# Kernel optimization log

Measured on AMD Instinct MI355X. Metric: run time of the kernel, lower is better.

The kernel has to match this reference:

```python
import jax, jax.numpy as jnp
import numpy as np

BATCH, NODE, IN_DIM, DIM, TOPK = 256, 256, 64, 64, 20
EPS = 1e-5
NEG_SLOPE = 0.2


def setup_inputs() -> dict:
    key = jax.random.key(0)
    ks = jax.random.split(key, 10)
    z, o = jnp.zeros, jnp.ones
    return {
        "data": jax.random.normal(ks[0], (BATCH, NODE, IN_DIM), jnp.float32),
        "emb_table": jax.random.normal(ks[1], (NODE, DIM), jnp.float32) * 0.1,
        "lin_w": jax.random.normal(ks[2], (IN_DIM, DIM), jnp.float32) * 0.05,
        "att_i": jax.random.normal(ks[3], (DIM,), jnp.float32) * 0.1,
        "att_j": jax.random.normal(ks[4], (DIM,), jnp.float32) * 0.1,
        "att_em_i": jax.random.normal(ks[5], (DIM,), jnp.float32) * 0.1,
        "att_em_j": jax.random.normal(ks[6], (DIM,), jnp.float32) * 0.1,
        "gnn_bias": z((DIM,), jnp.float32),
        "bn1_gamma": o((DIM,), jnp.float32), "bn1_beta": z((DIM,), jnp.float32),
        "bn2_gamma": o((DIM,), jnp.float32), "bn2_beta": z((DIM,), jnp.float32),
        "enc_w": jax.random.normal(ks[7], (NODE * DIM, DIM), jnp.float32) * 0.01,
        "enc_b": z((DIM,), jnp.float32),
        "arr_w": jax.random.normal(ks[8], (DIM, 7), jnp.float32) * 0.1,
        "arr_b": z((7,), jnp.float32),
        "out_w": jax.random.normal(ks[9], (DIM, 1), jnp.float32) * 0.1,
        "out_b": z((1,), jnp.float32),
    }


def _batchnorm(x, gamma, beta, axes):
    # BatchNorm1d in training mode: batch statistics
    mean = jnp.mean(x, axis=axes, keepdims=True)
    var = jnp.var(x, axis=axes, keepdims=True)
    return (x - mean) * jax.lax.rsqrt(var + EPS) * gamma + beta


def _gdn_forward(data, emb_table, lin_w, att_i, att_j, att_em_i, att_em_j, gnn_bias,
                 bn1_gamma, bn1_beta, bn2_gamma, bn2_beta,
                 enc_w, enc_b, arr_w, arr_b, out_w, out_b):
    B, N, F = data.shape
    BN = B * N
    x = data.reshape(BN, F)

    # learned graph: top-k cosine similarity of (detached) node embeddings
    w = jax.lax.stop_gradient(emb_table)
    nrm = jnp.linalg.norm(w, axis=-1)
    cos = (w @ w.T) / (nrm[:, None] * nrm[None, :])
    topk_idx = jax.lax.top_k(cos, TOPK)[1]                 # [N, TOPK]

    # gated_edge_index = (gated_j=sources, gated_i=targets), batched with +b*N offset
    src1 = topk_idx.reshape(-1)                            # sources (j)
    dst1 = jnp.repeat(jnp.arange(N), TOPK)                 # targets (i)
    offs = (jnp.arange(B) * N)[:, None]
    src = (src1[None, :] + offs).reshape(-1)               # [B*N*TOPK]
    dst = (dst1[None, :] + offs).reshape(-1)

    # PyG: remove_self_loops then add_self_loops -> mask duplicate self edges,
    # append exactly one self loop per node
    loop = jnp.arange(BN)
    src_all = jnp.concatenate([src, loop])
    dst_all = jnp.concatenate([dst, loop])
    valid = jnp.concatenate([src != dst, jnp.ones((BN,), bool)])

    # GraphLayer (GAT-style, heads=1, concat=False)
    xl = x @ lin_w                                         # [BN, DIM]
    emb_rep = jnp.tile(emb_table, (B, 1))                  # [BN, DIM] (embedding.repeat(B,1))
    x_i, x_j = xl[dst_all], xl[src_all]                    # per-edge gathers
    e_i, e_j = emb_rep[dst_all], emb_rep[src_all]
    logits = (x_i @ att_i) + (e_i @ att_em_i) + (x_j @ att_j) + (e_j @ att_em_j)
    logits = jnp.where(logits >= 0, logits, NEG_SLOPE * logits)  # leaky_relu(0.2)
    logits = jnp.where(valid, logits, -1e9)

    # segment softmax over incoming edges of each target node
    seg_max = jax.ops.segment_max(logits, dst_all, num_segments=BN)
    a = jnp.where(valid, jnp.exp(logits - seg_max[dst_all]), 0.0)
    denom = jax.ops.segment_sum(a, dst_all, num_segments=BN)
    alpha = a / denom[dst_all]

    # weighted scatter-add aggregation + bias, then GNNLayer BN + ReLU
    agg = jax.ops.segment_sum(x_j * alpha[:, None], dst_all, num_segments=BN) + gnn_bias
    gnn_out = jax.nn.relu(_batchnorm(agg, bn1_gamma, bn1_beta, axes=(0,)))

    x3 = gnn_out.reshape(B, N, -1)                         # [B, N, DIM]
    encoded = x3.reshape(B, -1) @ enc_w + enc_b            # [B, DIM]
    arrangement = encoded @ arr_w + arr_b                  # [B, 7]

    y = x3 * emb_table[None]                               # mul by node embeddings
    y = jnp.transpose(y, (0, 2, 1))                        # [B, DIM, N]
    y = jax.nn.relu(_batchnorm(y, bn2_gamma[None, :, None], bn2_beta[None, :, None], axes=(0, 2)))
    y = jnp.transpose(y, (0, 2, 1))                        # [B, N, DIM] (dropout is identity in eval)
    score = (y @ out_w + out_b).reshape(B, N)              # OutLayer (layer_num=1) + view(-1, N)
    return score, arrangement


def reference(data, emb_table, lin_w, att_i, att_j, att_em_i, att_em_j, gnn_bias,
              bn1_gamma, bn1_beta, bn2_gamma, bn2_beta,
              enc_w, enc_b, arr_w, arr_b, out_w, out_b):
    return _gdn_forward(data, emb_table, lin_w, att_i, att_j, att_em_i, att_em_j, gnn_bias,
                        bn1_gamma, bn1_beta, bn2_gamma, bn2_beta,
                        enc_w, enc_b, arr_w, arr_b, out_w, out_b)
```

## Files before the change

### kernel.cpp

```cpp
#include <hip/hip_runtime.h>
#include <hip/hip_bf16.h>

#define TK 20
#define BN 65536

typedef const float* fpc;
typedef __attribute__((ext_vector_type(8))) short short8;
typedef __attribute__((ext_vector_type(4))) float floatx4;

__device__ __forceinline__ short f2b(float f){
  unsigned u = __float_as_uint(f);
  return (short)((u + 0x7fffu + ((u >> 16) & 1u)) >> 16);
}
__device__ __forceinline__ float b2fu(unsigned short u){
  return __uint_as_float(((unsigned)u) << 16);
}

__global__ void __launch_bounds__(256) k_gx(fpc data, fpc emb, fpc lin_w, fpc att_i, fpc att_j,
        fpc att_em_i, fpc att_em_j,
        int* __restrict__ topk, float* __restrict__ emi, float* __restrict__ emj,
        __hip_bfloat16* __restrict__ xl, float* __restrict__ aip, float* __restrict__ ajp,
        float* __restrict__ bnsum){
  __shared__ float s_cos[256];
  __shared__ float s_wi[64];
  const int t = threadIdx.x, w = t >> 6, lane = t & 63;

  if (blockIdx.x < 256){
    if (blockIdx.x == 0){
      #pragma unroll
      for (int i = 0; i < 8; ++i) bnsum[t + i*256] = 0.f;
    }
    const int i = blockIdx.x;
    if (t < 64) s_wi[t] = emb[i*64 + t];
    __syncthreads();
    float dot = 0.f, nj = 0.f, ni = 0.f;
    for (int f = 0; f < 64; ++f){
      float wj = emb[t*64 + f], wi = s_wi[f];
      dot = fmaf(wi, wj, dot); nj = fmaf(wj, wj, nj); ni = fmaf(wi, wi, ni);
    }
    s_cos[t] = dot / (sqrtf(ni) * sqrtf(nj));
    __syncthreads();
    if (t < 64){
      float v0 = s_cos[t], v1 = s_cos[t+64], v2 = s_cos[t+128], v3 = s_cos[t+192];
      int taken = 0;
      for (int r = 0; r < TK; ++r){
        float bv = (taken & 1) ? -3.f : v0; int bi = t;
        float c;
        c = (taken & 2) ? -3.f : v1; if (c > bv){ bv = c; bi = t+64;  }
        c = (taken & 4) ? -3.f : v2; if (c > bv){ bv = c; bi = t+128; }
        c = (taken & 8) ? -3.f : v3; if (c > bv){ bv = c; bi = t+192; }
        for (int m = 1; m < 64; m <<= 1){
          float ov = __shfl_xor(bv, m, 64);
          int   oi = __shfl_xor(bi, m, 64);
          if (ov > bv || (ov == bv && oi < bi)){ bv = ov; bi = oi; }
        }
        if (t == 0) topk[i*TK + r] = bi;
        if ((bi & 63) == t) taken |= 1 << (bi >> 6);
      }
    } else if (t < 128){
      int d = t - 64;
      float wv = s_wi[d];
      float p1 = wv * att_em_i[d];
      float p2 = wv * att_em_j[d];
      for (int m = 1; m < 64; m <<= 1){
        p1 += __shfl_xor(p1, m, 64);
        p2 += __shfl_xor(p2, m, 64);
      }
      if (d == 0){ emi[i] = p1; emj[i] = p2; }
    }
    return;
  }

  const int m = lane & 15, quad = lane >> 4;
  short8 B[4][2];
  #pragma unroll
  for (int ct = 0; ct < 4; ++ct)
    #pragma unroll
    for (int kc = 0; kc < 2; ++kc)
      #pragma unroll
      for (int j = 0; j < 8; ++j)
        B[ct][kc][j] = f2b(lin_w[(kc*32 + quad*8 + j)*64 + ct*16 + m]);

  const int rw = (blockIdx.x - 256)*64 + w*16;
  short8 A0, A1;
  {
    const float4* ap0 = (const float4*)(data + (size_t)(rw + m)*64 + quad*8);
    float4 q0 = ap0[0], q1 = ap0[1];
    A0[0]=f2b(q0.x); A0[1]=f2b(q0.y); A0[2]=f2b(q0.z); A0[3]=f2b(q0.w);
    A0[4]=f2b(q1.x); A0[5]=f2b(q1.y); A0[6]=f2b(q1.z); A0[7]=f2b(q1.w);
    const float4* ap1 = (const float4*)(data + (size_t)(rw + m)*64 + 32 + quad*8);
    float4 q2 = ap1[0], q3 = ap1[1];
    A1[0]=f2b(q2.x); A1[1]=f2b(q2.y); A1[2]=f2b(q2.z); A1[3]=f2b(q2.w);
    A1[4]=f2b(q3.x); A1[5]=f2b(q3.y); A1[6]=f2b(q3.z); A1[7]=f2b(q3.w);
  }
  floatx4 acc[4];
  #pragma unroll
  for (int ct = 0; ct < 4; ++ct){
    floatx4 z = {0.f, 0.f, 0.f, 0.f};
    acc[ct] = __builtin_amdgcn_mfma_f32_16x16x32_bf16(A0, B[ct][0], z, 0, 0, 0);
    acc[ct] = __builtin_amdgcn_mfma_f32_16x16x32_bf16(A1, B[ct][1], acc[ct], 0, 0, 0);
  }
  float p1[4] = {0.f,0.f,0.f,0.f}, p2[4] = {0.f,0.f,0.f,0.f};
  #pragma unroll
  for (int ct = 0; ct < 4; ++ct){
    const float wi = att_i[ct*16 + m], wj = att_j[ct*16 + m];
    #pragma unroll
    for (int reg = 0; reg < 4; ++reg){
      float v = acc[ct][reg];
      const int row = rw + quad*4 + reg;
      xl[(size_t)row*64 + ct*16 + m] = __float2bfloat16(v);
      p1[reg] = fmaf(v, wi, p1[reg]);
      p2[reg] = fmaf(v, wj, p2[reg]);
    }
  }
  #pragma unroll
  for (int reg = 0; reg < 4; ++reg){
    #pragma unroll
    for (int s = 1; s < 16; s <<= 1){
      p1[reg] += __shfl_xor(p1[reg], s, 16);
      p2[reg] += __shfl_xor(p2[reg], s, 16);
    }
    if (m == 0){
      const int r = rw + quad*4 + reg;
      aip[r] = p1[reg];
      ajp[r] = p2[reg];
    }
  }
}

__global__ void __launch_bounds__(256) k_attn_agg(const int* __restrict__ topk,
                         const __hip_bfloat16* __restrict__ xl,
                         fpc aip, fpc ajp, fpc emi_g, fpc emj_g, fpc gnn_bias,
                         __hip_bfloat16* __restrict__ agg, float* __restrict__ bnsum){
  __shared__ float s_alpha[4][32];
  __shared__ int   s_src[4][32];
  __shared__ float s_ps[4][64], s_pq[4][64];
  const int t = threadIdx.x, w = t >> 6, lane = t & 63;
  const float bias = gnn_bias[lane];
  const int vbase = blockIdx.x*64 + w*16;
  float sum = 0.f, sq = 0.f;
  for (int j = 0; j < 16; ++j){
    const int v = vbase + j, i = v & 255, b = v >> 8;
    float lg = -1e30f; int sl = 0;
    if (lane < 21){
      sl = (lane < 20) ? topk[i*TK + lane] : i;
      if (lane == 20 || sl != i){
        float l = aip[v] + emi_g[i] + ajp[b*256 + sl] + emj_g[sl];
        lg = (l >= 0.f) ? l : 0.2f*l;
      }
    }
    float m = lg;
    for (int s = 1; s < 32; s <<= 1) m = fmaxf(m, __shfl_xor(m, s, 32));
    float e = (lg > -1e29f) ? __expf(lg - m) : 0.f;
    float den = e;
    for (int s = 1; s < 32; s <<= 1) den += __shfl_xor(den, s, 32);
    if (lane < 21){ s_alpha[w][lane] = e / den; s_src[w][lane] = b*256 + sl; }
    float acc = bias;
    #pragma unroll
    for (int k = 0; k < 21; ++k)
      acc = fmaf(s_alpha[w][k], __bfloat162float(xl[(size_t)s_src[w][k]*64 + lane]), acc);
    agg[(size_t)v*64 + lane] = __float2bfloat16(acc);
    sum += acc; sq = fmaf(acc, acc, sq);
  }
  s_ps[w][lane] = sum; s_pq[w][lane] = sq;
  __syncthreads();
  if (t < 64){
    const int cp = (blockIdx.x & 7)*64;
    atomicAdd(&bnsum[cp + t],       s_ps[0][t] + s_ps[1][t] + s_ps[2][t] + s_ps[3][t]);
    atomicAdd(&bnsum[512 + cp + t], s_pq[0][t] + s_pq[1][t] + s_pq[2][t] + s_pq[3][t]);
  }
}

__global__ void __launch_bounds__(256) k_encst(const __hip_bfloat16* __restrict__ agg, fpc enc_w,
                         fpc emb, fpc g1, fpc be1,
                         float* __restrict__ bnsum, float* __restrict__ part){
  const int t = threadIdx.x;

  if (blockIdx.x < 256){
    const int w = t >> 6, lane = t & 63;
    const int m = lane & 15, quad = lane >> 4;
    const int kt = blockIdx.x & 127, bt = blockIdx.x >> 7, kbase = kt*128;
    float scA[8], shA[8], scB[8], shB[8];
    #pragma unroll
    for (int j = 0; j < 8; ++j){
      #pragma unroll
      for (int par = 0; par < 2; ++par){
        const int d = par*32 + quad*8 + j;
        float S = 0.f, Q = 0.f;
        #pragma unroll
        for (int cp = 0; cp < 8; ++cp){ S += bnsum[cp*64 + d]; Q += bnsum[512 + cp*64 + d]; }
        float mean = S * (1.f/BN);
        float var  = Q * (1.f/BN) - mean*mean;
        float sc = g1[d] * rsqrtf(var + 1e-5f);
        float sh = be1[d] - mean*sc;
        if (par == 0){ scA[j] = sc; shA[j] = sh; } else { scB[j] = sc; shB[j] = sh; }
      }
    }
    floatx4 acc[2][4];
    #pragma unroll
    for (int i = 0; i < 2; ++i)
      #pragma unroll
      for (int ct = 0; ct < 4; ++ct)
        acc[i][ct] = (floatx4){0.f, 0.f, 0.f, 0.f};

    #pragma unroll
    for (int kc = 0; kc < 4; ++kc){
      const int kof = kbase + kc*32 + quad*8;
      const bool odd = (kc & 1);
      short8 Bf[4];
      #pragma unroll
      for (int ct = 0; ct < 4; ++ct)
        #pragma unroll
        for (int j = 0; j < 8; ++j)
          Bf[ct][j] = f2b(enc_w[(size_t)(kof + j)*64 + ct*16 + m]);
      #pragma unroll
      for (int i = 0; i < 2; ++i){
        const int row = bt*128 + (w*2 + i)*16 + m;
        uint4 uu = *(const uint4*)((const unsigned short*)agg + (size_t)row*16384 + kof);
        unsigned short h[8] = {
          (unsigned short)(uu.x & 0xffff), (unsigned short)(uu.x >> 16),
          (unsigned short)(uu.y & 0xffff), (unsigned short)(uu.y >> 16),
          (unsigned short)(uu.z & 0xffff), (unsigned short)(uu.z >> 16),
          (unsigned short)(uu.w & 0xffff), (unsigned short)(uu.w >> 16) };
        short8 Af;
        if (!odd){
          #pragma unroll
          for (int j = 0; j < 8; ++j) Af[j] = f2b(fmaxf(fmaf(b2fu(h[j]), scA[j], shA[j]), 0.f));
        } else {
          #pragma unroll
          for (int j = 0; j < 8; ++j) Af[j] = f2b(fmaxf(fmaf(b2fu(h[j]), scB[j], shB[j]), 0.f));
        }
        #pragma unroll
        for (int ct = 0; ct < 4; ++ct)
          acc[i][ct] = __builtin_amdgcn_mfma_f32_16x16x32_bf16(Af, Bf[ct], acc[i][ct], 0, 0, 0);
      }
    }
    #pragma unroll
    for (int i = 0; i < 2; ++i)
      #pragma unroll
      for (int ct = 0; ct < 4; ++ct)
        #pragma unroll
        for (int reg = 0; reg < 4; ++reg){
          const int row = bt*128 + (w*2 + i)*16 + quad*4 + reg;
          part[(size_t)kt*16384 + row*64 + ct*16 + m] = acc[i][ct][reg];
        }
    return;
  }

  const int sb = blockIdx.x - 256;
  const int qc = t & 15, rs = t >> 4;
  float4 sc, sh;
  {
    float s[4], q[4];
    #pragma unroll
    for (int k = 0; k < 4; ++k){
      const int d = qc*4 + k;
      float S = 0.f, Q = 0.f;
      #pragma unroll
      for (int cp = 0; cp < 8; ++cp){ S += bnsum[cp*64 + d]; Q += bnsum[512 + cp*64 + d]; }
      float mean = S * (1.f/BN);
      float var  = Q * (1.f/BN) - mean*mean;
      s[k] = g1[d] * rsqrtf(var + 1e-5f);
      q[k] = be1[d] - mean*s[k];
    }
    sc = make_float4(s[0], s[1], s[2], s[3]);
    sh = make_float4(q[0], q[1], q[2], q[3]);
  }
  const float4* emb4 = (const float4*)emb;
  float4 ys = make_float4(0,0,0,0), yq = make_float4(0,0,0,0);
  const int rbase = sb*32;
  #pragma unroll
  for (int jj = 0; jj < 2; ++jj){
    const int r = rbase + jj*16 + rs;
    ushort4 u = *(const ushort4*)((const unsigned short*)agg + (size_t)r*64 + qc*4);
    float4 e = emb4[(r & 255)*16 + qc];
    float4 y;
    y.x = fmaxf(fmaf(b2fu(u.x), sc.x, sh.x), 0.f) * e.x;
    y.y = fmaxf(fmaf(b2fu(u.y), sc.y, sh.y), 0.f) * e.y;
    y.z = fmaxf(fmaf(b2fu(u.z), sc.z, sh.z), 0.f) * e.z;
    y.w = fmaxf(fmaf(b2fu(u.w), sc.w, sh.w), 0.f) * e.w;
    ys.x += y.x; ys.y += y.y; ys.z += y.z; ys.w += y.w;
    yq.x = fmaf(y.x, y.x, yq.x); yq.y = fmaf(y.y, y.y, yq.y);
    yq.z = fmaf(y.z, y.z, yq.z); yq.w = fmaf(y.w, y.w, yq.w);
  }
  __shared__ float4 s_s[16][16], s_q[16][16];
  s_s[rs][qc] = ys; s_q[rs][qc] = yq;
  __syncthreads();
  if (t < 64){
    const int qq = t >> 2, comp = t & 3;
    float S = 0.f, Q = 0.f;
    #pragma unroll
    for (int rr = 0; rr < 16; ++rr){
      S += ((const float*)&s_s[rr][qq])[comp];
      Q += ((const float*)&s_q[rr][qq])[comp];
    }
    const int cp = (sb & 7)*64;
    atomicAdd(&bnsum[1024 + cp + t], S);
    atomicAdd(&bnsum[1536 + cp + t], Q);
  }
}

__global__ void __launch_bounds__(256) k_fin(const float* __restrict__ part,
                      const __hip_bfloat16* __restrict__ agg, fpc emb,
                      fpc g1, fpc be1, fpc g2, fpc be2,
                      const float* __restrict__ bnsum,
                      fpc enc_b, fpc arr_w, fpc arr_b, fpc out_w, fpc out_b,
                      float* __restrict__ out){
  const int t = threadIdx.x;

  if (blockIdx.x < 256){
    __shared__ float s_enc[4][64];
    const int b = blockIdx.x, w = t >> 6, lane = t & 63;
    float s = 0.f;
    #pragma unroll 8
    for (int k = 0; k < 32; ++k)
      s += part[(size_t)(w*32 + k)*16384 + b*64 + lane];
    s_enc[w][lane] = s;
    __syncthreads();
    if (t < 64){
      float e = s_enc[0][t] + s_enc[1][t] + s_enc[2][t] + s_enc[3][t] + enc_b[t];
      float o[7];
      #pragma unroll
      for (int j = 0; j < 7; ++j) o[j] = e * arr_w[t*7 + j];
      #pragma unroll
      for (int j = 0; j < 7; ++j)
        #pragma unroll
        for (int m = 1; m < 64; m <<= 1) o[j] += __shfl_xor(o[j], m, 64);
      if (t == 0){
        #pragma unroll
        for (int j = 0; j < 7; ++j) out[65536 + b*7 + j] = o[j] + arr_b[j];
      }
    }
    return;
  }

  const int w = t >> 6, lane = t & 63;
  const int qc = lane & 15, rq = lane >> 4;
  float sc1[4], sh1[4], sc2[4], sh2[4], ow[4];
  #pragma unroll
  for (int k = 0; k < 4; ++k){
    const int d = qc*4 + k;
    float S1 = 0.f, Q1 = 0.f, S2 = 0.f, Q2 = 0.f;
    #pragma unroll
    for (int cp = 0; cp < 8; ++cp){
      S1 += bnsum[cp*64 + d];        Q1 += bnsum[512 + cp*64 + d];
      S2 += bnsum[1024 + cp*64 + d]; Q2 += bnsum[1536 + cp*64 + d];
    }
    float m1 = S1 * (1.f/BN), v1 = Q1 * (1.f/BN) - m1*m1;
    sc1[k] = g1[d] * rsqrtf(v1 + 1e-5f);
    sh1[k] = be1[d] - m1*sc1[k];
    float m2 = S2 * (1.f/BN), v2 = Q2 * (1.f/BN) - m2*m2;
    sc2[k] = g2[d] * rsqrtf(v2 + 1e-5f);
    sh2[k] = be2[d] - m2*sc2[k];
    ow[k]  = out_w[d];
  }
  const float ob = out_b[0];
  const float4* emb4 = (const float4*)emb;
  const int base = (blockIdx.x - 256)*32 + w*8;
  #pragma unroll
  for (int it = 0; it < 2; ++it){
    const int r = base + it*4 + rq;
    ushort4 u = *(const ushort4*)((const unsigned short*)agg + (size_t)r*64 + qc*4);
    float4 e4 = emb4[(r & 255)*16 + qc];
    float p = 0.f, g, y, yh;
    g = fmaxf(fmaf(b2fu(u.x), sc1[0], sh1[0]), 0.f); y = g*e4.x;
    yh = fmaxf(fmaf(y, sc2[0], sh2[0]), 0.f); p = fmaf(yh, ow[0], p);
    g = fmaxf(fmaf(b2fu(u.y), sc1[1], sh1[1]), 0.f); y = g*e4.y;
    yh = fmaxf(fmaf(y, sc2[1], sh2[1]), 0.f); p = fmaf(yh, ow[1], p);
    g = fmaxf(fmaf(b2fu(u.z), sc1[2], sh1[2]), 0.f); y = g*e4.z;
    yh = fmaxf(fmaf(y, sc2[2], sh2[2]), 0.f); p = fmaf(yh, ow[2], p);
    g = fmaxf(fmaf(b2fu(u.w), sc1[3], sh1[3]), 0.f); y = g*e4.w;
    yh = fmaxf(fmaf(y, sc2[3], sh2[3]), 0.f); p = fmaf(yh, ow[3], p);
    #pragma unroll
    for (int mm = 1; mm < 16; mm <<= 1) p += __shfl_xor(p, mm, 16);
    if (qc == 0) out[r] = p + ob;
  }
}

extern "C" void kernel_launch(void* const* d_in, const int* in_sizes, int n_in,
                              void* d_out, int out_size, void* d_ws, size_t ws_size,
                              hipStream_t stream) {
  fpc data     = (fpc)d_in[0];
  fpc emb      = (fpc)d_in[1];
  fpc lin_w    = (fpc)d_in[2];
  fpc att_i    = (fpc)d_in[3];
  fpc att_j    = (fpc)d_in[4];
  fpc att_em_i = (fpc)d_in[5];
  fpc att_em_j = (fpc)d_in[6];
  fpc gnn_bias = (fpc)d_in[7];
  fpc g1       = (fpc)d_in[8];
  fpc be1      = (fpc)d_in[9];
  fpc g2       = (fpc)d_in[10];
  fpc be2      = (fpc)d_in[11];
  fpc enc_w    = (fpc)d_in[12];
  fpc enc_b    = (fpc)d_in[13];
  fpc arr_w    = (fpc)d_in[14];
  fpc arr_b    = (fpc)d_in[15];
  fpc out_w    = (fpc)d_in[16];
  fpc out_b    = (fpc)d_in[17];

  float* fw = (float*)d_ws;
  int*   topk    = (int*)d_ws;
  float* emi     = fw + 5120;
  float* emj     = fw + 5376;
  float* bnsum   = fw + 5632;
  float* aip     = fw + 7680;
  float* ajp     = fw + 73216;
  __hip_bfloat16* agg = (__hip_bfloat16*)(fw + 138752);
  __hip_bfloat16* xl  = (__hip_bfloat16*)(fw + 2235904);
  float* part    = (float*)xl;
  float* out     = (float*)d_out;

  k_gx       <<<1280,  256, 0, stream>>>(data, emb, lin_w, att_i, att_j, att_em_i, att_em_j,
                                         topk, emi, emj, xl, aip, ajp, bnsum);
  k_attn_agg <<<1024,  256, 0, stream>>>(topk, xl, aip, ajp, emi, emj, gnn_bias, agg, bnsum);
  k_encst    <<<2304,  256, 0, stream>>>(agg, enc_w, emb, g1, be1, bnsum, part);
  k_fin      <<<2304,  256, 0, stream>>>(part, agg, emb, g1, be1, g2, be2, bnsum,
                                         enc_b, arr_w, arr_b, out_w, out_b, out);
}
```

Measured before the change: 174.4 us.

## Fuse four kernels into one persistent kernel with grid-wide barriers

```diff
diff --git a/kernel.cpp b/kernel.cpp
--- a/kernel.cpp
+++ b/kernel.cpp
@@ -3,6 +3,7 @@
 
 #define TK 20
 #define BN 65536
+#define NB 512
 
 typedef const float* fpc;
 typedef __attribute__((ext_vector_type(8))) short short8;
@@ -16,26 +17,49 @@
   return __uint_as_float(((unsigned)u) << 16);
 }
 
-__global__ void __launch_bounds__(256) k_gx(fpc data, fpc emb, fpc lin_w, fpc att_i, fpc att_j,
-        fpc att_em_i, fpc att_em_j,
-        int* __restrict__ topk, float* __restrict__ emi, float* __restrict__ emj,
-        __hip_bfloat16* __restrict__ xl, float* __restrict__ aip, float* __restrict__ ajp,
-        float* __restrict__ bnsum){
+struct KP {
+  const float *data, *emb, *lin_w, *att_i, *att_j, *att_em_i, *att_em_j,
+              *gnn_bias, *g1, *be1, *g2, *be2, *enc_w, *enc_b, *arr_w, *arr_b,
+              *out_w, *out_b;
+  int *topk;
+  float *emi, *emj, *bnsum;
+  unsigned *bar;
+  float *aip, *ajp;
+  __hip_bfloat16 *agg, *xl;
+  float *part, *out;
+};
+
+__device__ __forceinline__ void gbar(unsigned* bar, unsigned target){
+  __syncthreads();
+  if (threadIdx.x == 0){
+    __threadfence();
+    __hip_atomic_fetch_add(bar, 1u, __ATOMIC_RELEASE, __HIP_MEMORY_SCOPE_AGENT);
+    while (__hip_atomic_load(bar, __ATOMIC_ACQUIRE, __HIP_MEMORY_SCOPE_AGENT) < target)
+      __builtin_amdgcn_s_sleep(8);
+    __threadfence();
+  }
+  __syncthreads();
+}
+
+__global__ void __launch_bounds__(256, 2) mega(KP p){
+  const int t = threadIdx.x, w = t >> 6, lane = t & 63;
+  const int m = lane & 15, quad = lane >> 4;
+
   __shared__ float s_cos[256];
   __shared__ float s_wi[64];
-  const int t = threadIdx.x, w = t >> 6, lane = t & 63;
+  __shared__ float s_alpha[4][32];
+  __shared__ int   s_src[4][32];
+  __shared__ float s_ps[4][64], s_pq[4][64];
+  __shared__ float4 s_s[16][16], s_q[16][16];
+  __shared__ float s_enc[4][64];
 
   if (blockIdx.x < 256){
-    if (blockIdx.x == 0){
-      #pragma unroll
-      for (int i = 0; i < 8; ++i) bnsum[t + i*256] = 0.f;
-    }
     const int i = blockIdx.x;
-    if (t < 64) s_wi[t] = emb[i*64 + t];
+    if (t < 64) s_wi[t] = p.emb[i*64 + t];
     __syncthreads();
     float dot = 0.f, nj = 0.f, ni = 0.f;
     for (int f = 0; f < 64; ++f){
-      float wj = emb[t*64 + f], wi = s_wi[f];
+      float wj = p.emb[t*64 + f], wi = s_wi[f];
       dot = fmaf(wi, wj, dot); nj = fmaf(wj, wj, nj); ni = fmaf(wi, wi, ni);
     }
     s_cos[t] = dot / (sqrtf(ni) * sqrtf(nj));
@@ -49,136 +73,125 @@
         c = (taken & 2) ? -3.f : v1; if (c > bv){ bv = c; bi = t+64;  }
         c = (taken & 4) ? -3.f : v2; if (c > bv){ bv = c; bi = t+128; }
         c = (taken & 8) ? -3.f : v3; if (c > bv){ bv = c; bi = t+192; }
-        for (int m = 1; m < 64; m <<= 1){
-          float ov = __shfl_xor(bv, m, 64);
-          int   oi = __shfl_xor(bi, m, 64);
+        for (int mm = 1; mm < 64; mm <<= 1){
+          float ov = __shfl_xor(bv, mm, 64);
+          int   oi = __shfl_xor(bi, mm, 64);
           if (ov > bv || (ov == bv && oi < bi)){ bv = ov; bi = oi; }
         }
-        if (t == 0) topk[i*TK + r] = bi;
+        if (t == 0) p.topk[i*TK + r] = bi;
         if ((bi & 63) == t) taken |= 1 << (bi >> 6);
       }
     } else if (t < 128){
       int d = t - 64;
       float wv = s_wi[d];
-      float p1 = wv * att_em_i[d];
-      float p2 = wv * att_em_j[d];
-      for (int m = 1; m < 64; m <<= 1){
-        p1 += __shfl_xor(p1, m, 64);
-        p2 += __shfl_xor(p2, m, 64);
-      }
-      if (d == 0){ emi[i] = p1; emj[i] = p2; }
-    }
-    return;
-  }
-
-  const int m = lane & 15, quad = lane >> 4;
-  short8 B[4][2];
-  #pragma unroll
-  for (int ct = 0; ct < 4; ++ct)
-    #pragma unroll
-    for (int kc = 0; kc < 2; ++kc)
-      #pragma unroll
-      for (int j = 0; j < 8; ++j)
-        B[ct][kc][j] = f2b(lin_w[(kc*32 + quad*8 + j)*64 + ct*16 + m]);
-
-  const int rw = (blockIdx.x - 256)*64 + w*16;
-  short8 A0, A1;
+      float p1 = wv * p.att_em_i[d];
+      float p2 = wv * p.att_em_j[d];
+      for (int mm = 1; mm < 64; mm <<= 1){
+        p1 += __shfl_xor(p1, mm, 64);
+        p2 += __shfl_xor(p2, mm, 64);
+      }
+      if (d == 0){ p.emi[i] = p1; p.emj[i] = p2; }
+    }
+    __syncthreads();
+  }
   {
-    const float4* ap0 = (const float4*)(data + (size_t)(rw + m)*64 + quad*8);
-    float4 q0 = ap0[0], q1 = ap0[1];
-    A0[0]=f2b(q0.x); A0[1]=f2b(q0.y); A0[2]=f2b(q0.z); A0[3]=f2b(q0.w);
-    A0[4]=f2b(q1.x); A0[5]=f2b(q1.y); A0[6]=f2b(q1.z); A0[7]=f2b(q1.w);
-    const float4* ap1 = (const float4*)(data + (size_t)(rw + m)*64 + 32 + quad*8);
-    float4 q2 = ap1[0], q3 = ap1[1];
-    A1[0]=f2b(q2.x); A1[1]=f2b(q2.y); A1[2]=f2b(q2.z); A1[3]=f2b(q2.w);
-    A1[4]=f2b(q3.x); A1[5]=f2b(q3.y); A1[6]=f2b(q3.z); A1[7]=f2b(q3.w);
-  }
-  floatx4 acc[4];
-  #pragma unroll
-  for (int ct = 0; ct < 4; ++ct){
-    floatx4 z = {0.f, 0.f, 0.f, 0.f};
-    acc[ct] = __builtin_amdgcn_mfma_f32_16x16x32_bf16(A0, B[ct][0], z, 0, 0, 0);
-    acc[ct] = __builtin_amdgcn_mfma_f32_16x16x32_bf16(A1, B[ct][1], acc[ct], 0, 0, 0);
-  }
-  float p1[4] = {0.f,0.f,0.f,0.f}, p2[4] = {0.f,0.f,0.f,0.f};
-  #pragma unroll
-  for (int ct = 0; ct < 4; ++ct){
-    const float wi = att_i[ct*16 + m], wj = att_j[ct*16 + m];
-    #pragma unroll
-    for (int reg = 0; reg < 4; ++reg){
-      float v = acc[ct][reg];
-      const int row = rw + quad*4 + reg;
-      xl[(size_t)row*64 + ct*16 + m] = __float2bfloat16(v);
-      p1[reg] = fmaf(v, wi, p1[reg]);
-      p2[reg] = fmaf(v, wj, p2[reg]);
-    }
-  }
-  #pragma unroll
-  for (int reg = 0; reg < 4; ++reg){
-    #pragma unroll
-    for (int s = 1; s < 16; s <<= 1){
-      p1[reg] += __shfl_xor(p1[reg], s, 16);
-      p2[reg] += __shfl_xor(p2[reg], s, 16);
-    }
-    if (m == 0){
-      const int r = rw + quad*4 + reg;
-      aip[r] = p1[reg];
-      ajp[r] = p2[reg];
-    }
-  }
-}
-
-__global__ void __launch_bounds__(256) k_attn_agg(const int* __restrict__ topk,
-                         const __hip_bfloat16* __restrict__ xl,
-                         fpc aip, fpc ajp, fpc emi_g, fpc emj_g, fpc gnn_bias,
-                         __hip_bfloat16* __restrict__ agg, float* __restrict__ bnsum){
-  __shared__ float s_alpha[4][32];
-  __shared__ int   s_src[4][32];
-  __shared__ float s_ps[4][64], s_pq[4][64];
-  const int t = threadIdx.x, w = t >> 6, lane = t & 63;
-  const float bias = gnn_bias[lane];
-  const int vbase = blockIdx.x*64 + w*16;
-  float sum = 0.f, sq = 0.f;
-  for (int j = 0; j < 16; ++j){
-    const int v = vbase + j, i = v & 255, b = v >> 8;
-    float lg = -1e30f; int sl = 0;
-    if (lane < 21){
-      sl = (lane < 20) ? topk[i*TK + lane] : i;
-      if (lane == 20 || sl != i){
-        float l = aip[v] + emi_g[i] + ajp[b*256 + sl] + emj_g[sl];
-        lg = (l >= 0.f) ? l : 0.2f*l;
-      }
-    }
-    float m = lg;
-    for (int s = 1; s < 32; s <<= 1) m = fmaxf(m, __shfl_xor(m, s, 32));
-    float e = (lg > -1e29f) ? __expf(lg - m) : 0.f;
-    float den = e;
-    for (int s = 1; s < 32; s <<= 1) den += __shfl_xor(den, s, 32);
-    if (lane < 21){ s_alpha[w][lane] = e / den; s_src[w][lane] = b*256 + sl; }
-    float acc = bias;
-    #pragma unroll
-    for (int k = 0; k < 21; ++k)
-      acc = fmaf(s_alpha[w][k], __bfloat162float(xl[(size_t)s_src[w][k]*64 + lane]), acc);
-    agg[(size_t)v*64 + lane] = __float2bfloat16(acc);
-    sum += acc; sq = fmaf(acc, acc, sq);
-  }
-  s_ps[w][lane] = sum; s_pq[w][lane] = sq;
-  __syncthreads();
-  if (t < 64){
-    const int cp = (blockIdx.x & 7)*64;
-    atomicAdd(&bnsum[cp + t],       s_ps[0][t] + s_ps[1][t] + s_ps[2][t] + s_ps[3][t]);
-    atomicAdd(&bnsum[512 + cp + t], s_pq[0][t] + s_pq[1][t] + s_pq[2][t] + s_pq[3][t]);
-  }
-}
-
-__global__ void __launch_bounds__(256) k_encst(const __hip_bfloat16* __restrict__ agg, fpc enc_w,
-                         fpc emb, fpc g1, fpc be1,
-                         float* __restrict__ bnsum, float* __restrict__ part){
-  const int t = threadIdx.x;
-
-  if (blockIdx.x < 256){
-    const int w = t >> 6, lane = t & 63;
-    const int m = lane & 15, quad = lane >> 4;
+    short8 B[4][2];
+    #pragma unroll
+    for (int ct = 0; ct < 4; ++ct)
+      #pragma unroll
+      for (int kc = 0; kc < 2; ++kc)
+        #pragma unroll
+        for (int j = 0; j < 8; ++j)
+          B[ct][kc][j] = f2b(p.lin_w[(kc*32 + quad*8 + j)*64 + ct*16 + m]);
+    #pragma unroll
+    for (int pass = 0; pass < 2; ++pass){
+      const int rw = blockIdx.x*128 + pass*64 + w*16;
+      short8 A0, A1;
+      {
+        const float4* ap0 = (const float4*)(p.data + (size_t)(rw + m)*64 + quad*8);
+        float4 q0 = ap0[0], q1 = ap0[1];
+        A0[0]=f2b(q0.x); A0[1]=f2b(q0.y); A0[2]=f2b(q0.z); A0[3]=f2b(q0.w);
+        A0[4]=f2b(q1.x); A0[5]=f2b(q1.y); A0[6]=f2b(q1.z); A0[7]=f2b(q1.w);
+        const float4* ap1 = (const float4*)(p.data + (size_t)(rw + m)*64 + 32 + quad*8);
+        float4 q2 = ap1[0], q3 = ap1[1];
+        A1[0]=f2b(q2.x); A1[1]=f2b(q2.y); A1[2]=f2b(q2.z); A1[3]=f2b(q2.w);
+        A1[4]=f2b(q3.x); A1[5]=f2b(q3.y); A1[6]=f2b(q3.z); A1[7]=f2b(q3.w);
+      }
+      floatx4 acc[4];
+      #pragma unroll
+      for (int ct = 0; ct < 4; ++ct){
+        floatx4 z = {0.f, 0.f, 0.f, 0.f};
+        acc[ct] = __builtin_amdgcn_mfma_f32_16x16x32_bf16(A0, B[ct][0], z, 0, 0, 0);
+        acc[ct] = __builtin_amdgcn_mfma_f32_16x16x32_bf16(A1, B[ct][1], acc[ct], 0, 0, 0);
+      }
+      float p1[4] = {0.f,0.f,0.f,0.f}, p2[4] = {0.f,0.f,0.f,0.f};
+      #pragma unroll
+      for (int ct = 0; ct < 4; ++ct){
+        const float wi = p.att_i[ct*16 + m], wj = p.att_j[ct*16 + m];
+        #pragma unroll
+        for (int reg = 0; reg < 4; ++reg){
+          float v = acc[ct][reg];
+          const int row = rw + quad*4 + reg;
+          p.xl[(size_t)row*64 + ct*16 + m] = __float2bfloat16(v);
+          p1[reg] = fmaf(v, wi, p1[reg]);
+          p2[reg] = fmaf(v, wj, p2[reg]);
+        }
+      }
+      #pragma unroll
+      for (int reg = 0; reg < 4; ++reg){
+        #pragma unroll
+        for (int s = 1; s < 16; s <<= 1){
+          p1[reg] += __shfl_xor(p1[reg], s, 16);
+          p2[reg] += __shfl_xor(p2[reg], s, 16);
+        }
+        if (m == 0){
+          const int r = rw + quad*4 + reg;
+          p.aip[r] = p1[reg];
+          p.ajp[r] = p2[reg];
+        }
+      }
+    }
+  }
+  gbar(p.bar, NB);
+
+  {
+    const float bias = p.gnn_bias[lane];
+    const int vbase = blockIdx.x*128 + w*32;
+    float sum = 0.f, sq = 0.f;
+    for (int j = 0; j < 32; ++j){
+      const int v = vbase + j, i = v & 255, b = v >> 8;
+      float lg = -1e30f; int sl = 0;
+      if (lane < 21){
+        sl = (lane < 20) ? p.topk[i*TK + lane] : i;
+        if (lane == 20 || sl != i){
+          float l = p.aip[v] + p.emi[i] + p.ajp[b*256 + sl] + p.emj[sl];
+          lg = (l >= 0.f) ? l : 0.2f*l;
+        }
+      }
+      float mx = lg;
+      for (int s = 1; s < 32; s <<= 1) mx = fmaxf(mx, __shfl_xor(mx, s, 32));
+      float e = (lg > -1e29f) ? __expf(lg - mx) : 0.f;
+      float den = e;
+      for (int s = 1; s < 32; s <<= 1) den += __shfl_xor(den, s, 32);
+      if (lane < 21){ s_alpha[w][lane] = e / den; s_src[w][lane] = b*256 + sl; }
+      float acc = bias;
+      #pragma unroll
+      for (int k = 0; k < 21; ++k)
+        acc = fmaf(s_alpha[w][k], __bfloat162float(p.xl[(size_t)s_src[w][k]*64 + lane]), acc);
+      p.agg[(size_t)v*64 + lane] = __float2bfloat16(acc);
+      sum += acc; sq = fmaf(acc, acc, sq);
+    }
+    s_ps[w][lane] = sum; s_pq[w][lane] = sq;
+    __syncthreads();
+    if (t < 64){
+      const int cp = (blockIdx.x & 7)*64;
+      atomicAdd(&p.bnsum[cp + t],       s_ps[0][t] + s_ps[1][t] + s_ps[2][t] + s_ps[3][t]);
+      atomicAdd(&p.bnsum[512 + cp + t], s_pq[0][t] + s_pq[1][t] + s_pq[2][t] + s_pq[3][t]);
+    }
+  }
+  gbar(p.bar, 2*NB);
+
+  {
     const int kt = blockIdx.x & 127, bt = blockIdx.x >> 7, kbase = kt*128;
     float scA[8], shA[8], scB[8], shB[8];
     #pragma unroll
@@ -188,21 +201,17 @@
         const int d = par*32 + quad*8 + j;
         float S = 0.f, Q = 0.f;
         #pragma unroll
-        for (int cp = 0; cp < 8; ++cp){ S += bnsum[cp*64 + d]; Q += bnsum[512 + cp*64 + d]; }
+        for (int cp = 0; cp < 8; ++cp){ S += p.bnsum[cp*64 + d]; Q += p.bnsum[512 + cp*64 + d]; }
         float mean = S * (1.f/BN);
         float var  = Q * (1.f/BN) - mean*mean;
-        float sc = g1[d] * rsqrtf(var + 1e-5f);
-        float sh = be1[d] - mean*sc;
+        float sc = p.g1[d] * rsqrtf(var + 1e-5f);
+        float sh = p.be1[d] - mean*sc;
         if (par == 0){ scA[j] = sc; shA[j] = sh; } else { scB[j] = sc; shB[j] = sh; }
       }
     }
-    floatx4 acc[2][4];
-    #pragma unroll
-    for (int i = 0; i < 2; ++i)
-      #pragma unroll
-      for (int ct = 0; ct < 4; ++ct)
-        acc[i][ct] = (floatx4){0.f, 0.f, 0.f, 0.f};
-
+    floatx4 acc[4];
+    #pragma unroll
+    for (int ct = 0; ct < 4; ++ct) acc[ct] = (floatx4){0.f, 0.f, 0.f, 0.f};
     #pragma unroll
     for (int kc = 0; kc < 4; ++kc){
       const int kof = kbase + kc*32 + quad*8;
@@ -212,209 +221,191 @@
       for (int ct = 0; ct < 4; ++ct)
         #pragma unroll
         for (int j = 0; j < 8; ++j)
-          Bf[ct][j] = f2b(enc_w[(size_t)(kof + j)*64 + ct*16 + m]);
-      #pragma unroll
-      for (int i = 0; i < 2; ++i){
-        const int row = bt*128 + (w*2 + i)*16 + m;
-        uint4 uu = *(const uint4*)((const unsigned short*)agg + (size_t)row*16384 + kof);
-        unsigned short h[8] = {
-          (unsigned short)(uu.x & 0xffff), (unsigned short)(uu.x >> 16),
-          (unsigned short)(uu.y & 0xffff), (unsigned short)(uu.y >> 16),
-          (unsigned short)(uu.z & 0xffff), (unsigned short)(uu.z >> 16),
-          (unsigned short)(uu.w & 0xffff), (unsigned short)(uu.w >> 16) };
-        short8 Af;
-        if (!odd){
-          #pragma unroll
-          for (int j = 0; j < 8; ++j) Af[j] = f2b(fmaxf(fmaf(b2fu(h[j]), scA[j], shA[j]), 0.f));
-        } else {
-          #pragma unroll
-          for (int j = 0; j < 8; ++j) Af[j] = f2b(fmaxf(fmaf(b2fu(h[j]), scB[j], shB[j]), 0.f));
-        }
-        #pragma unroll
-        for (int ct = 0; ct < 4; ++ct)
-          acc[i][ct] = __builtin_amdgcn_mfma_f32_16x16x32_bf16(Af, Bf[ct], acc[i][ct], 0, 0, 0);
-      }
-    }
-    #pragma unroll
-    for (int i = 0; i < 2; ++i)
+          Bf[ct][j] = f2b(p.enc_w[(size_t)(kof + j)*64 + ct*16 + m]);
+      const int row = bt*64 + w*16 + m;
+      uint4 uu = *(const uint4*)((const unsigned short*)p.agg + (size_t)row*16384 + kof);
+      unsigned short h[8] = {
+        (unsigned short)(uu.x & 0xffff), (unsigned short)(uu.x >> 16),
+        (unsigned short)(uu.y & 0xffff), (unsigned short)(uu.y >> 16),
+        (unsigned short)(uu.z & 0xffff), (unsigned short)(uu.z >> 16),
+        (unsigned short)(uu.w & 0xffff), (unsigned short)(uu.w >> 16) };
+      short8 Af;
+      if (!odd){
+        #pragma unroll
+        for (int j = 0; j < 8; ++j) Af[j] = f2b(fmaxf(fmaf(b2fu(h[j]), scA[j], shA[j]), 0.f));
+      } else {
+        #pragma unroll
+        for (int j = 0; j < 8; ++j) Af[j] = f2b(fmaxf(fmaf(b2fu(h[j]), scB[j], shB[j]), 0.f));
+      }
       #pragma unroll
       for (int ct = 0; ct < 4; ++ct)
-        #pragma unroll
-        for (int reg = 0; reg < 4; ++reg){
-          const int row = bt*128 + (w*2 + i)*16 + quad*4 + reg;
-          part[(size_t)kt*16384 + row*64 + ct*16 + m] = acc[i][ct][reg];
-        }
-    return;
-  }
-
-  const int sb = blockIdx.x - 256;
-  const int qc = t & 15, rs = t >> 4;
-  float4 sc, sh;
+        acc[ct] = __builtin_amdgcn_mfma_f32_16x16x32_bf16(Af, Bf[ct], acc[ct], 0, 0, 0);
+    }
+    #pragma unroll
+    for (int ct = 0; ct < 4; ++ct)
+      #pragma unroll
+      for (int reg = 0; reg < 4; ++reg){
+        const int row = bt*64 + w*16 + quad*4 + reg;
+        p.part[(size_t)kt*16384 + row*64 + ct*16 + m] = acc[ct][reg];
+      }
+  }
   {
-    float s[4], q[4];
-    #pragma unroll
-    for (int k = 0; k < 4; ++k){
-      const int d = qc*4 + k;
+    const int qc = t & 15, rs = t >> 4;
+    float4 sc, sh;
+    {
+      float s[4], q[4];
+      #pragma unroll
+      for (int k = 0; k < 4; ++k){
+        const int d = qc*4 + k;
+        float S = 0.f, Q = 0.f;
+        #pragma unroll
+        for (int cp = 0; cp < 8; ++cp){ S += p.bnsum[cp*64 + d]; Q += p.bnsum[512 + cp*64 + d]; }
+        float mean = S * (1.f/BN);
+        float var  = Q * (1.f/BN) - mean*mean;
+        s[k] = p.g1[d] * rsqrtf(var + 1e-5f);
+        q[k] = p.be1[d] - mean*s[k];
+      }
+      sc = make_float4(s[0], s[1], s[2], s[3]);
+      sh = make_float4(q[0], q[1], q[2], q[3]);
+    }
+    const float4* emb4 = (const float4*)p.emb;
+    float4 ys = make_float4(0,0,0,0), yq = make_float4(0,0,0,0);
+    const int rbase = blockIdx.x*128;
+    #pragma unroll
+    for (int jj = 0; jj < 8; ++jj){
+      const int r = rbase + jj*16 + rs;
+      ushort4 u = *(const ushort4*)((const unsigned short*)p.agg + (size_t)r*64 + qc*4);
+      float4 e = emb4[(r & 255)*16 + qc];
+      float4 y;
+      y.x = fmaxf(fmaf(b2fu(u.x), sc.x, sh.x), 0.f) * e.x;
+      y.y = fmaxf(fmaf(b2fu(u.y), sc.y, sh.y), 0.f) * e.y;
+      y.z = fmaxf(fmaf(b2fu(u.z), sc.z, sh.z), 0.f) * e.z;
+      y.w = fmaxf(fmaf(b2fu(u.w), sc.w, sh.w), 0.f) * e.w;
+      ys.x += y.x; ys.y += y.y; ys.z += y.z; ys.w += y.w;
+      yq.x = fmaf(y.x, y.x, yq.x); yq.y = fmaf(y.y, y.y, yq.y);
+      yq.z = fmaf(y.z, y.z, yq.z); yq.w = fmaf(y.w, y.w, yq.w);
+    }
+    s_s[rs][qc] = ys; s_q[rs][qc] = yq;
+    __syncthreads();
+    if (t < 64){
+      const int qq = t >> 2, comp = t & 3;
       float S = 0.f, Q = 0.f;
       #pragma unroll
-      for (int cp = 0; cp < 8; ++cp){ S += bnsum[cp*64 + d]; Q += bnsum[512 + cp*64 + d]; }
-      float mean = S * (1.f/BN);
-      float var  = Q * (1.f/BN) - mean*mean;
-      s[k] = g1[d] * rsqrtf(var + 1e-5f);
-      q[k] = be1[d] - mean*s[k];
-    }
-    sc = make_float4(s[0], s[1], s[2], s[3]);
-    sh = make_float4(q[0], q[1], q[2], q[3]);
-  }
-  const float4* emb4 = (const float4*)emb;
-  float4 ys = make_float4(0,0,0,0), yq = make_float4(0,0,0,0);
-  const int rbase = sb*32;
-  #pragma unroll
-  for (int jj = 0; jj < 2; ++jj){
-    const int r = rbase + jj*16 + rs;
-    ushort4 u = *(const ushort4*)((const unsigned short*)agg + (size_t)r*64 + qc*4);
-    float4 e = emb4[(r & 255)*16 + qc];
-    float4 y;
-    y.x = fmaxf(fmaf(b2fu(u.x), sc.x, sh.x), 0.f) * e.x;
-    y.y = fmaxf(fmaf(b2fu(u.y), sc.y, sh.y), 0.f) * e.y;
-    y.z = fmaxf(fmaf(b2fu(u.z), sc.z, sh.z), 0.f) * e.z;
-    y.w = fmaxf(fmaf(b2fu(u.w), sc.w, sh.w), 0.f) * e.w;
-    ys.x += y.x; ys.y += y.y; ys.z += y.z; ys.w += y.w;
-    yq.x = fmaf(y.x, y.x, yq.x); yq.y = fmaf(y.y, y.y, yq.y);
-    yq.z = fmaf(y.z, y.z, yq.z); yq.w = fmaf(y.w, y.w, yq.w);
-  }
-  __shared__ float4 s_s[16][16], s_q[16][16];
-  s_s[rs][qc] = ys; s_q[rs][qc] = yq;
-  __syncthreads();
-  if (t < 64){
-    const int qq = t >> 2, comp = t & 3;
-    float S = 0.f, Q = 0.f;
-    #pragma unroll
-    for (int rr = 0; rr < 16; ++rr){
-      S += ((const float*)&s_s[rr][qq])[comp];
-      Q += ((const float*)&s_q[rr][qq])[comp];
-    }
-    const int cp = (sb & 7)*64;
-    atomicAdd(&bnsum[1024 + cp + t], S);
-    atomicAdd(&bnsum[1536 + cp + t], Q);
-  }
-}
-
-__global__ void __launch_bounds__(256) k_fin(const float* __restrict__ part,
-                      const __hip_bfloat16* __restrict__ agg, fpc emb,
-                      fpc g1, fpc be1, fpc g2, fpc be2,
-                      const float* __restrict__ bnsum,
-                      fpc enc_b, fpc arr_w, fpc arr_b, fpc out_w, fpc out_b,
-                      float* __restrict__ out){
-  const int t = threadIdx.x;
+      for (int rr = 0; rr < 16; ++rr){
+        S += ((const float*)&s_s[rr][qq])[comp];
+        Q += ((const float*)&s_q[rr][qq])[comp];
+      }
+      const int cp = (blockIdx.x & 7)*64;
+      atomicAdd(&p.bnsum[1024 + cp + t], S);
+      atomicAdd(&p.bnsum[1536 + cp + t], Q);
+    }
+  }
+  gbar(p.bar, 3*NB);
 
   if (blockIdx.x < 256){
-    __shared__ float s_enc[4][64];
-    const int b = blockIdx.x, w = t >> 6, lane = t & 63;
+    const int b = blockIdx.x;
     float s = 0.f;
     #pragma unroll 8
     for (int k = 0; k < 32; ++k)
-      s += part[(size_t)(w*32 + k)*16384 + b*64 + lane];
+      s += p.part[(size_t)(w*32 + k)*16384 + b*64 + lane];
     s_enc[w][lane] = s;
     __syncthreads();
     if (t < 64){
-      float e = s_enc[0][t] + s_enc[1][t] + s_enc[2][t] + s_enc[3][t] + enc_b[t];
+      float e = s_enc[0][t] + s_enc[1][t] + s_enc[2][t] + s_enc[3][t] + p.enc_b[t];
       float o[7];
       #pragma unroll
-      for (int j = 0; j < 7; ++j) o[j] = e * arr_w[t*7 + j];
+      for (int j = 0; j < 7; ++j) o[j] = e * p.arr_w[t*7 + j];
       #pragma unroll
       for (int j = 0; j < 7; ++j)
         #pragma unroll
-        for (int m = 1; m < 64; m <<= 1) o[j] += __shfl_xor(o[j], m, 64);
+        for (int mm = 1; mm < 64; mm <<= 1) o[j] += __shfl_xor(o[j], mm, 64);
       if (t == 0){
         #pragma unroll
-        for (int j = 0; j < 7; ++j) out[65536 + b*7 + j] = o[j] + arr_b[j];
-      }
-    }
-    return;
-  }
-
-  const int w = t >> 6, lane = t & 63;
-  const int qc = lane & 15, rq = lane >> 4;
-  float sc1[4], sh1[4], sc2[4], sh2[4], ow[4];
-  #pragma unroll
-  for (int k = 0; k < 4; ++k){
-    const int d = qc*4 + k;
-    float S1 = 0.f, Q1 = 0.f, S2 = 0.f, Q2 = 0.f;
-    #pragma unroll
-    for (int cp = 0; cp < 8; ++cp){
-      S1 += bnsum[cp*64 + d];        Q1 += bnsum[512 + cp*64 + d];
-      S2 += bnsum[1024 + cp*64 + d]; Q2 += bnsum[1536 + cp*64 + d];
-    }
-    float m1 = S1 * (1.f/BN), v1 = Q1 * (1.f/BN) - m1*m1;
-    sc1[k] = g1[d] * rsqrtf(v1 + 1e-5f);
-    sh1[k] = be1[d] - m1*sc1[k];
-    float m2 = S2 * (1.f/BN), v2 = Q2 * (1.f/BN) - m2*m2;
-    sc2[k] = g2[d] * rsqrtf(v2 + 1e-5f);
-    sh2[k] = be2[d] - m2*sc2[k];
-    ow[k]  = out_w[d];
-  }
-  const float ob = out_b[0];
-  const float4* emb4 = (const float4*)emb;
-  const int base = (blockIdx.x - 256)*32 + w*8;
-  #pragma unroll
-  for (int it = 0; it < 2; ++it){
-    const int r = base + it*4 + rq;
-    ushort4 u = *(const ushort4*)((const unsigned short*)agg + (size_t)r*64 + qc*4);
-    float4 e4 = emb4[(r & 255)*16 + qc];
-    float p = 0.f, g, y, yh;
-    g = fmaxf(fmaf(b2fu(u.x), sc1[0], sh1[0]), 0.f); y = g*e4.x;
-    yh = fmaxf(fmaf(y, sc2[0], sh2[0]), 0.f); p = fmaf(yh, ow[0], p);
-    g = fmaxf(fmaf(b2fu(u.y), sc1[1], sh1[1]), 0.f); y = g*e4.y;
-    yh = fmaxf(fmaf(y, sc2[1], sh2[1]), 0.f); p = fmaf(yh, ow[1], p);
-    g = fmaxf(fmaf(b2fu(u.z), sc1[2], sh1[2]), 0.f); y = g*e4.z;
-    yh = fmaxf(fmaf(y, sc2[2], sh2[2]), 0.f); p = fmaf(yh, ow[2], p);
-    g = fmaxf(fmaf(b2fu(u.w), sc1[3], sh1[3]), 0.f); y = g*e4.w;
-    yh = fmaxf(fmaf(y, sc2[3], sh2[3]), 0.f); p = fmaf(yh, ow[3], p);
-    #pragma unroll
-    for (int mm = 1; mm < 16; mm <<= 1) p += __shfl_xor(p, mm, 16);
-    if (qc == 0) out[r] = p + ob;
+        for (int j = 0; j < 7; ++j) p.out[65536 + b*7 + j] = o[j] + p.arr_b[j];
+      }
+    }
+    __syncthreads();
+  }
+  {
+    const int qc = lane & 15, rq = lane >> 4;
+    float sc1[4], sh1[4], sc2[4], sh2[4], ow[4];
+    #pragma unroll
+    for (int k = 0; k < 4; ++k){
+      const int d = qc*4 + k;
+      float S1 = 0.f, Q1 = 0.f, S2 = 0.f, Q2 = 0.f;
+      #pragma unroll
+      for (int cp = 0; cp < 8; ++cp){
+        S1 += p.bnsum[cp*64 + d];        Q1 += p.bnsum[512 + cp*64 + d];
+        S2 += p.bnsum[1024 + cp*64 + d]; Q2 += p.bnsum[1536 + cp*64 + d];
+      }
+      float m1 = S1 * (1.f/BN), v1 = Q1 * (1.f/BN) - m1*m1;
+      sc1[k] = p.g1[d] * rsqrtf(v1 + 1e-5f);
+      sh1[k] = p.be1[d] - m1*sc1[k];
+      float m2 = S2 * (1.f/BN), v2 = Q2 * (1.f/BN) - m2*m2;
+      sc2[k] = p.g2[d] * rsqrtf(v2 + 1e-5f);
+      sh2[k] = p.be2[d] - m2*sc2[k];
+      ow[k]  = p.out_w[d];
+    }
+    const float ob = p.out_b[0];
+    const float4* emb4 = (const float4*)p.emb;
+    const int base = blockIdx.x*128 + w*32;
+    #pragma unroll
+    for (int it = 0; it < 8; ++it){
+      const int r = base + it*4 + rq;
+      ushort4 u = *(const ushort4*)((const unsigned short*)p.agg + (size_t)r*64 + qc*4);
+      float4 e4 = emb4[(r & 255)*16 + qc];
+      float pr = 0.f, g, y, yh;
+      g = fmaxf(fmaf(b2fu(u.x), sc1[0], sh1[0]), 0.f); y = g*e4.x;
+      yh = fmaxf(fmaf(y, sc2[0], sh2[0]), 0.f); pr = fmaf(yh, ow[0], pr);
+      g = fmaxf(fmaf(b2fu(u.y), sc1[1], sh1[1]), 0.f); y = g*e4.y;
+      yh = fmaxf(fmaf(y, sc2[1], sh2[1]), 0.f); pr = fmaf(yh, ow[1], pr);
+      g = fmaxf(fmaf(b2fu(u.z), sc1[2], sh1[2]), 0.f); y = g*e4.z;
+      yh = fmaxf(fmaf(y, sc2[2], sh2[2]), 0.f); pr = fmaf(yh, ow[2], pr);
+      g = fmaxf(fmaf(b2fu(u.w), sc1[3], sh1[3]), 0.f); y = g*e4.w;
+      yh = fmaxf(fmaf(y, sc2[3], sh2[3]), 0.f); pr = fmaf(yh, ow[3], pr);
+      #pragma unroll
+      for (int mm = 1; mm < 16; mm <<= 1) pr += __shfl_xor(pr, mm, 16);
+      if (qc == 0) p.out[r] = pr + ob;
+    }
   }
 }
 
 extern "C" void kernel_launch(void* const* d_in, const int* in_sizes, int n_in,
                               void* d_out, int out_size, void* d_ws, size_t ws_size,
                               hipStream_t stream) {
-  fpc data     = (fpc)d_in[0];
-  fpc emb      = (fpc)d_in[1];
-  fpc lin_w    = (fpc)d_in[2];
-  fpc att_i    = (fpc)d_in[3];
-  fpc att_j    = (fpc)d_in[4];
-  fpc att_em_i = (fpc)d_in[5];
-  fpc att_em_j = (fpc)d_in[6];
-  fpc gnn_bias = (fpc)d_in[7];
-  fpc g1       = (fpc)d_in[8];
-  fpc be1      = (fpc)d_in[9];
-  fpc g2       = (fpc)d_in[10];
-  fpc be2      = (fpc)d_in[11];
-  fpc enc_w    = (fpc)d_in[12];
-  fpc enc_b    = (fpc)d_in[13];
-  fpc arr_w    = (fpc)d_in[14];
-  fpc arr_b    = (fpc)d_in[15];
-  fpc out_w    = (fpc)d_in[16];
-  fpc out_b    = (fpc)d_in[17];
+  KP p;
+  p.data     = (fpc)d_in[0];
+  p.emb      = (fpc)d_in[1];
+  p.lin_w    = (fpc)d_in[2];
+  p.att_i    = (fpc)d_in[3];
+  p.att_j    = (fpc)d_in[4];
+  p.att_em_i = (fpc)d_in[5];
+  p.att_em_j = (fpc)d_in[6];
+  p.gnn_bias = (fpc)d_in[7];
+  p.g1       = (fpc)d_in[8];
+  p.be1      = (fpc)d_in[9];
+  p.g2       = (fpc)d_in[10];
+  p.be2      = (fpc)d_in[11];
+  p.enc_w    = (fpc)d_in[12];
+  p.enc_b    = (fpc)d_in[13];
+  p.arr_w    = (fpc)d_in[14];
+  p.arr_b    = (fpc)d_in[15];
+  p.out_w    = (fpc)d_in[16];
+  p.out_b    = (fpc)d_in[17];
 
   float* fw = (float*)d_ws;
-  int*   topk    = (int*)d_ws;
-  float* emi     = fw + 5120;
-  float* emj     = fw + 5376;
-  float* bnsum   = fw + 5632;
-  float* aip     = fw + 7680;
-  float* ajp     = fw + 73216;
-  __hip_bfloat16* agg = (__hip_bfloat16*)(fw + 138752);
-  __hip_bfloat16* xl  = (__hip_bfloat16*)(fw + 2235904);
-  float* part    = (float*)xl;
-  float* out     = (float*)d_out;
-
-  k_gx       <<<1280,  256, 0, stream>>>(data, emb, lin_w, att_i, att_j, att_em_i, att_em_j,
-                                         topk, emi, emj, xl, aip, ajp, bnsum);
-  k_attn_agg <<<1024,  256, 0, stream>>>(topk, xl, aip, ajp, emi, emj, gnn_bias, agg, bnsum);
-  k_encst    <<<2304,  256, 0, stream>>>(agg, enc_w, emb, g1, be1, bnsum, part);
-  k_fin      <<<2304,  256, 0, stream>>>(part, agg, emb, g1, be1, g2, be2, bnsum,
-                                         enc_b, arr_w, arr_b, out_w, out_b, out);
+  p.topk  = (int*)d_ws;
+  p.emi   = fw + 5120;
+  p.emj   = fw + 5376;
+  p.bnsum = fw + 5632;
+  p.bar   = (unsigned*)(fw + 7680);
+  p.aip   = fw + 7744;
+  p.ajp   = fw + 73280;
+  p.agg   = (__hip_bfloat16*)(fw + 138816);
+  p.xl    = (__hip_bfloat16*)(fw + 2235968);
+  p.part  = (float*)p.xl;
+  p.out   = (float*)d_out;
+
+  hipMemsetAsync((void*)p.bnsum, 0, 2112u*sizeof(float), stream);
+  mega<<<NB, 256, 0, stream>>>(p);
 }
```

Result: slower. 403.3 us (+131.2%).
